# Kernel tuning notes

Hardware: AMD Instinct MI355X
Metric: run time of the kernel (lower is better)

The kernel has to match this reference:

```python
import jax, jax.numpy as jnp
import numpy as np

EPS = 1e-8

def rms_norm(x, scale):
    # norm(2,-1)/sqrt(d); x / (rms + eps) * scale
    d = x.shape[-1]
    norm = jnp.sqrt(jnp.sum(x * x, axis=-1, keepdims=True))
    rms = norm / jnp.sqrt(jnp.asarray(d, x.dtype))
    return scale * (x / (rms + EPS))

def setup_inputs() -> dict:
    key = jax.random.key(0)
    B, N, C, FF = 2, 2048, 1024, 4096
    ks = jax.random.split(key, 12)
    s = 0.02
    return {
        "x":  jax.random.normal(ks[0], (B, N, C), jnp.float32),
        "wq": jax.random.normal(ks[1], (C, C), jnp.float32) * s,
        "bq": jnp.zeros((C,), jnp.float32),
        "wk": jax.random.normal(ks[2], (C, C), jnp.float32) * s,
        "bk": jnp.zeros((C,), jnp.float32),
        "wv": jax.random.normal(ks[3], (C, C), jnp.float32) * s,
        "bv": jnp.zeros((C,), jnp.float32),
        "wo": jax.random.normal(ks[4], (C, C), jnp.float32) * s,
        "bo": jnp.zeros((C,), jnp.float32),
        "scale1": jnp.ones((C,), jnp.float32),
        "scale2": jnp.ones((C,), jnp.float32),
        "w1": jax.random.normal(ks[5], (C, FF), jnp.float32) * s,
        "b1": jnp.zeros((FF,), jnp.float32),
        "w2": jax.random.normal(ks[6], (FF, C), jnp.float32) * s,
        "b2": jnp.zeros((C,), jnp.float32),
    }

def reference(x, wq, bq, wk, bk, wv, bv, wo, bo, scale1, scale2, w1, b1, w2, b2):
    B, N, C = x.shape
    H = 16
    D = C // H

    residual = x
    xn = rms_norm(x, scale1)

    def heads(y):  # [B,N,C] -> [B,H,N,D]
        return y.reshape(B, N, H, D).transpose(0, 2, 1, 3)

    q = heads(xn @ wq + bq)
    k = heads(xn @ wk + bk)
    v = heads(xn @ wv + bv)

    # apply_rotary_pos_emb with cos=sin=1: q' = q - roll(q,1,-1), same for k
    q = q - jnp.roll(q, 1, axis=-1)
    k = k - jnp.roll(k, 1, axis=-1)

    # explicit attention (no causal mask in original)
    scores = jnp.einsum('bhnd,bhmd->bhnm', q, k) / jnp.sqrt(jnp.asarray(D, x.dtype))
    probs = jax.nn.softmax(scores, axis=-1)
    attn = jnp.einsum('bhnm,bhmd->bhnd', probs, v)
    attn = attn.transpose(0, 2, 1, 3).reshape(B, N, C)
    attn = attn @ wo + bo

    x = residual + attn
    residual = x
    xn = rms_norm(x, scale2)
    h = jax.nn.gelu(xn @ w1 + b1, approximate=False)  # torch GELU default = exact
    ffn_out = h @ w2 + b2
    return residual + ffn_out
```

## Files before the change

### kernel.cpp

```cpp
#include <hip/hip_runtime.h>
#include <hip/hip_bf16.h>
#include <math.h>

typedef unsigned short u16;
typedef short s16x8 __attribute__((ext_vector_type(8)));
typedef __bf16 bf16x8v __attribute__((ext_vector_type(8)));
typedef float f32x4 __attribute__((ext_vector_type(4)));
typedef unsigned short u16x4 __attribute__((ext_vector_type(4)));

struct Ptr4 { float* p[4]; };
struct TW6 {
    const float* w[6]; u16* o[6]; int mode[6];
    const float *bq, *bk, *bv; float* bqkv;
};

__device__ __forceinline__ u16 f2b(float f) {
    __hip_bfloat16 h = __float2bfloat16(f);
    return __builtin_bit_cast(u16, h);
}

__device__ __forceinline__ f32x4 mfma16(s16x8 a, s16x8 b, f32x4 c) {
    return __builtin_amdgcn_mfma_f32_16x16x32_bf16(
        __builtin_bit_cast(bf16x8v, a), __builtin_bit_cast(bf16x8v, b), c, 0, 0, 0);
}

__device__ __forceinline__ void gl_lds16(const void* g, void* l) {
    typedef const unsigned int __attribute__((address_space(1))) * gp_t;
    typedef unsigned int __attribute__((address_space(3))) * lp_t;
    __builtin_amdgcn_global_load_lds((gp_t)(unsigned long long)g,
                                     (lp_t)(unsigned int)(unsigned long long)l,
                                     16, 0, 0);
}

__device__ __forceinline__ float gelu_fast(float v) {
    float u = 1.5957691216f * (v + 0.044715f * v * v * v);
    return v / (1.f + __expf(-u));
}

__global__ __launch_bounds__(256) void prep_weights(TW6 io) {
    const int z = blockIdx.z, bx = blockIdx.x, by = blockIdx.y;
    const float* W; u16* Wt; int mode = 0, N_, K_, n0, k0;
    if (z < 4) {
        if (bx >= 32) {
            if (z == 0 && bx < 44 && by == 0) {
                const int i = (bx - 32) * 256 + threadIdx.x;
                const int d = i & 1023;
                const int dp = (d & ~63) | ((d + 63) & 63);
                float v;
                if (i < 1024) v = 0.125f * (io.bq[d] - io.bq[dp]);
                else if (i < 2048) v = io.bk[d] - io.bk[dp];
                else v = io.bv[d];
                io.bqkv[i] = v;
            }
            return;
        }
        W = io.w[z]; Wt = io.o[z]; mode = io.mode[z];
        N_ = 1024; K_ = 1024; n0 = bx * 32; k0 = by * 32;
    } else if (z == 4) {
        W = io.w[4]; Wt = io.o[4]; N_ = 4096; K_ = 1024; n0 = bx * 32; k0 = by * 32;
    } else {
        W = io.w[5]; Wt = io.o[5]; N_ = 1024; K_ = 4096; n0 = by * 32; k0 = bx * 32;
    }
    __shared__ u16 tile[32][33];
    const int tx = threadIdx.x & 31, ty = threadIdx.x >> 5;
    const int n = n0 + tx;
    const int np = (n & ~63) | ((n + 63) & 63);
    const float s = (mode == 1) ? 0.125f : 1.f;
#pragma unroll
    for (int i = 0; i < 32; i += 8) {
        const size_t r = (size_t)(k0 + ty + i) * N_;
        float v = W[r + n];
        if (mode) v = (v - W[r + np]) * s;
        tile[ty + i][tx] = f2b(v);
    }
    __syncthreads();
#pragma unroll
    for (int i = 0; i < 32; i += 8)
        Wt[(size_t)(n0 + ty + i) * K_ + k0 + tx] = tile[tx][ty + i];
}

__global__ __launch_bounds__(256) void transpose_v(const u16* __restrict__ qkv,
                                                   u16* __restrict__ vT) {
    __shared__ u16 tile[32][33];
    const int tx = threadIdx.x & 31, ty = threadIdx.x >> 5;
    const int n0 = blockIdx.x * 32, d0 = blockIdx.y * 32, bh = blockIdx.z;
    const int b = bh >> 4, h = bh & 15;
#pragma unroll
    for (int i = 0; i < 32; i += 8)
        tile[ty + i][tx] =
            qkv[(size_t)(b * 2048 + n0 + ty + i) * 3072 + 2048 + h * 64 + d0 + tx];
    __syncthreads();
#pragma unroll
    for (int i = 0; i < 32; i += 8)
        vT[((size_t)bh * 64 + d0 + ty + i) * 2048 + n0 + tx] = tile[tx][ty + i];
}

__global__ __launch_bounds__(256) void rmsnorm_kernel(const float* __restrict__ x,
                                                      const float* __restrict__ scale,
                                                      u16* __restrict__ out) {
    __shared__ float red[4];
    const int t = threadIdx.x, row = blockIdx.x;
    const float4* xr = (const float4*)(x + (size_t)row * 1024);
    float4 v = xr[t];
    float ss = v.x * v.x + v.y * v.y + v.z * v.z + v.w * v.w;
#pragma unroll
    for (int off = 1; off < 64; off <<= 1) ss += __shfl_xor(ss, off);
    if ((t & 63) == 0) red[t >> 6] = ss;
    __syncthreads();
    float tot = red[0] + red[1] + red[2] + red[3];
    float inv = 1.f / (sqrtf(tot * (1.f / 1024.f)) + 1e-8f);
    const float4* sr = (const float4*)scale;
    float4 s = sr[t];
    u16x4 o;
    o[0] = f2b(v.x * inv * s.x);
    o[1] = f2b(v.y * inv * s.y);
    o[2] = f2b(v.z * inv * s.z);
    o[3] = f2b(v.w * inv * s.w);
    ((u16x4*)(out + (size_t)row * 1024))[t] = o;
}

template <int EPI>
__global__ __launch_bounds__(256) void gemm_kernel(const u16* __restrict__ A,
                                                   const u16* __restrict__ Bt,
                                                   const float* __restrict__ bias,
                                                   const float* __restrict__ resid,
                                                   void* __restrict__ outp,
                                                   int M, int N, int K) {
    __shared__ __align__(16) u16 As[128 * 64];
    __shared__ __align__(16) u16 Bs[128 * 64];
    const int t = threadIdx.x, lane = t & 63;
    const int w = t >> 6, wm = (w >> 1) * 64, wn = (w & 1) * 64;
    const int c = lane & 15, qd = lane >> 4;
    const int n0 = blockIdx.x * 128, m0 = blockIdx.y * 128;

    const int srow = t >> 3;
    const int sch8 = ((t & 7) ^ (srow & 7)) * 8;
    const u16* Ag = A + (size_t)(m0 + srow) * K + sch8;
    const u16* Bg = Bt + (size_t)(n0 + srow) * K + sch8;
    const size_t rstride = (size_t)32 * K;

    f32x4 acc[4][4] = {};
    for (int kt = 0; kt < K; kt += 64) {
        __syncthreads();
#pragma unroll
        for (int g = 0; g < 4; g++) {
            gl_lds16(Ag + g * rstride, &As[t * 8 + g * 2048]);
            gl_lds16(Bg + g * rstride, &Bs[t * 8 + g * 2048]);
        }
        Ag += 64;
        Bg += 64;
        __syncthreads();
#pragma unroll
        for (int s = 0; s < 2; s++) {
            s16x8 a[4], b[4];
#pragma unroll
            for (int im = 0; im < 4; im++)
                a[im] = *(const s16x8*)&As[(wm + im * 16 + c) * 64 +
                                           (((s * 4 + qd) ^ (c & 7)) * 8)];
#pragma unroll
            for (int jn = 0; jn < 4; jn++)
                b[jn] = *(const s16x8*)&Bs[(wn + jn * 16 + c) * 64 +
                                           (((s * 4 + qd) ^ (c & 7)) * 8)];
#pragma unroll
            for (int im = 0; im < 4; im++)
#pragma unroll
                for (int jn = 0; jn < 4; jn++)
                    acc[im][jn] = mfma16(a[im], b[jn], acc[im][jn]);
        }
    }

#pragma unroll
    for (int im = 0; im < 4; im++) {
#pragma unroll
        for (int jn = 0; jn < 4; jn++) {
            const int colg = n0 + wn + jn * 16 + c;
            const float bv = bias[colg];
#pragma unroll
            for (int r = 0; r < 4; r++) {
                const int rowg = m0 + wm + im * 16 + qd * 4 + r;
                const size_t off = (size_t)rowg * N + colg;
                float v = acc[im][jn][r] + bv;
                if (EPI == 0) {
                    ((u16*)outp)[off] = f2b(v);
                } else if (EPI == 1) {
                    ((float*)outp)[off] = v + resid[off];
                } else {
                    ((u16*)outp)[off] = f2b(gelu_fast(v));
                }
            }
        }
    }
}

__global__ __launch_bounds__(256) void gemm_splitk(const u16* __restrict__ A,
                                                   const u16* __restrict__ Bt,
                                                   Ptr4 parts,
                                                   int N, int Ktot, int Kc) {
    __shared__ __align__(16) u16 As[128 * 64];
    __shared__ __align__(16) u16 Bs[128 * 64];
    const int t = threadIdx.x, lane = t & 63;
    const int w = t >> 6, wm = (w >> 1) * 64, wn = (w & 1) * 64;
    const int c = lane & 15, qd = lane >> 4;
    const int n0 = blockIdx.x * 128, m0 = blockIdx.y * 128;
    const int z = blockIdx.z;
    float* out = parts.p[z];

    const int srow = t >> 3;
    const int sch8 = ((t & 7) ^ (srow & 7)) * 8;
    const u16* Ag = A + (size_t)(m0 + srow) * Ktot + z * Kc + sch8;
    const u16* Bg = Bt + (size_t)(n0 + srow) * Ktot + z * Kc + sch8;
    const size_t rstride = (size_t)32 * Ktot;

    f32x4 acc[4][4] = {};
    for (int kt = 0; kt < Kc; kt += 64) {
        __syncthreads();
#pragma unroll
        for (int g = 0; g < 4; g++) {
            gl_lds16(Ag + g * rstride, &As[t * 8 + g * 2048]);
            gl_lds16(Bg + g * rstride, &Bs[t * 8 + g * 2048]);
        }
        Ag += 64;
        Bg += 64;
        __syncthreads();
#pragma unroll
        for (int s = 0; s < 2; s++) {
            s16x8 a[4], b[4];
#pragma unroll
            for (int im = 0; im < 4; im++)
                a[im] = *(const s16x8*)&As[(wm + im * 16 + c) * 64 +
                                           (((s * 4 + qd) ^ (c & 7)) * 8)];
#pragma unroll
            for (int jn = 0; jn < 4; jn++)
                b[jn] = *(const s16x8*)&Bs[(wn + jn * 16 + c) * 64 +
                                           (((s * 4 + qd) ^ (c & 7)) * 8)];
#pragma unroll
            for (int im = 0; im < 4; im++)
#pragma unroll
                for (int jn = 0; jn < 4; jn++)
                    acc[im][jn] = mfma16(a[im], b[jn], acc[im][jn]);
        }
    }

#pragma unroll
    for (int im = 0; im < 4; im++)
#pragma unroll
        for (int jn = 0; jn < 4; jn++) {
            const int colg = n0 + wn + jn * 16 + c;
#pragma unroll
            for (int r = 0; r < 4; r++) {
                const int rowg = m0 + wm + im * 16 + qd * 4 + r;
                out[(size_t)rowg * N + colg] = acc[im][jn][r];
            }
        }
}

template <int S, bool NORM>
__global__ __launch_bounds__(256) void reduce_kernel(Ptr4 parts,
                                                     const float* __restrict__ bias,
                                                     const float* __restrict__ resid,
                                                     const float* __restrict__ scale,
                                                     float* __restrict__ yout,
                                                     u16* __restrict__ xnout) {
    __shared__ float red[4];
    const int t = threadIdx.x, row = blockIdx.x;
    const size_t base = (size_t)row * 1024;
    float4 v = ((const float4*)(resid + base))[t];
    float4 bv = ((const float4*)bias)[t];
    v.x += bv.x; v.y += bv.y; v.z += bv.z; v.w += bv.w;
#pragma unroll
    for (int s = 0; s < S; s++) {
        float4 pv = ((const float4*)(parts.p[s] + base))[t];
        v.x += pv.x; v.y += pv.y; v.z += pv.z; v.w += pv.w;
    }
    ((float4*)(yout + base))[t] = v;
    if (NORM) {
        float ss = v.x * v.x + v.y * v.y + v.z * v.z + v.w * v.w;
#pragma unroll
        for (int off = 1; off < 64; off <<= 1) ss += __shfl_xor(ss, off);
        if ((t & 63) == 0) red[t >> 6] = ss;
        __syncthreads();
        float tot = red[0] + red[1] + red[2] + red[3];
        float inv = 1.f / (sqrtf(tot * (1.f / 1024.f)) + 1e-8f);
        float4 s = ((const float4*)scale)[t];
        u16x4 o;
        o[0] = f2b(v.x * inv * s.x);
        o[1] = f2b(v.y * inv * s.y);
        o[2] = f2b(v.z * inv * s.z);
        o[3] = f2b(v.w * inv * s.w);
        ((u16x4*)(xnout + base))[t] = o;
    }
}

__global__ __launch_bounds__(256, 3) void attn_kernel(const u16* __restrict__ qkv,
                                                      const u16* __restrict__ vT,
                                                      u16* __restrict__ attn) {
    __shared__ __align__(16) u16 Ks[2][64 * 64];
    __shared__ __align__(16) u16 Vs[2][64 * 64];
    __shared__ __align__(16) u16 Ps[4 * 32 * 64];

    const int t = threadIdx.x, lane = t & 63, w = t >> 6;
    const int c = lane & 15, qd = lane >> 4;
    const int bh = blockIdx.y, b = bh >> 4, h = bh & 15;
    const int q0 = blockIdx.x * 128;
    const size_t rowbase = (size_t)b * 2048;

    const u16* kg = qkv + rowbase * 3072 + 1024 + h * 64;
    const u16* vg = vT + (size_t)bh * 64 * 2048;

    const int srow = t >> 3;
    const int sch = (t & 7) ^ (srow & 7);

    const u16* kptr = kg + (size_t)srow * 3072 + sch * 8;
    const u16* vptr = vg + (size_t)srow * 2048 + sch * 8;

    gl_lds16(kptr, &Ks[0][t * 8]);
    gl_lds16(kptr + (size_t)32 * 3072, &Ks[0][2048 + t * 8]);
    gl_lds16(vptr, &Vs[0][t * 8]);
    gl_lds16(vptr + (size_t)32 * 2048, &Vs[0][2048 + t * 8]);

    s16x8 qf[2][2];
    {
        const u16* qg = qkv + (rowbase + q0 + w * 32) * 3072 + h * 64;
#pragma unroll
        for (int im = 0; im < 2; im++)
#pragma unroll
            for (int ks = 0; ks < 2; ks++)
                qf[im][ks] = *(const s16x8*)&qg[(size_t)(im * 16 + c) * 3072 +
                                                ks * 32 + qd * 8];
    }
    __syncthreads();

    float lsum[2][4] = {};
    f32x4 o[2][4] = {};
    u16* Pw = &Ps[w * 32 * 64];

    for (int it = 0; it < 32; it++) {
        const int buf = it & 1;
        const u16* Kb = Ks[buf];
        const u16* Vb = Vs[buf];

        if (it + 1 < 32) {
            u16* Kn = Ks[buf ^ 1];
            u16* Vn = Vs[buf ^ 1];
            const size_t ko = (size_t)(it + 1) * 64 * 3072;
            const size_t vo = (size_t)(it + 1) * 64;
            gl_lds16(kptr + ko, &Kn[t * 8]);
            gl_lds16(kptr + ko + (size_t)32 * 3072, &Kn[2048 + t * 8]);
            gl_lds16(vptr + vo, &Vn[t * 8]);
            gl_lds16(vptr + vo + (size_t)32 * 2048, &Vn[2048 + t * 8]);
        }

        s16x8 kf[2][4], vf[2][4];
#pragma unroll
        for (int ks = 0; ks < 2; ks++)
#pragma unroll
            for (int j = 0; j < 4; j++) {
                const int rrow = j * 16 + c;
                const int sw = ((ks * 4 + qd) ^ (rrow & 7)) * 8;
                kf[ks][j] = *(const s16x8*)&Kb[rrow * 64 + sw];
                vf[ks][j] = *(const s16x8*)&Vb[rrow * 64 + sw];
            }

#pragma unroll
        for (int im = 0; im < 2; im++) {
            f32x4 sc[4] = {};
#pragma unroll
            for (int ks = 0; ks < 2; ks++)
#pragma unroll
                for (int jn = 0; jn < 4; jn++)
                    sc[jn] = mfma16(qf[im][ks], kf[ks][jn], sc[jn]);
#pragma unroll
            for (int r = 0; r < 4; r++) {
                const int prow = im * 16 + qd * 4 + r;
                float s = 0.f;
#pragma unroll
                for (int jn = 0; jn < 4; jn++) {
                    float p = __expf(sc[jn][r]);
                    s += p;
                    Pw[prow * 64 + (((jn * 2 + (c >> 3)) ^ (prow & 7)) * 8) + (c & 7)] =
                        f2b(p);
                }
                lsum[im][r] += s;
            }
        }

#pragma unroll
        for (int im = 0; im < 2; im++)
#pragma unroll
            for (int ks = 0; ks < 2; ks++) {
                s16x8 pf = *(const s16x8*)&Pw[(im * 16 + c) * 64 +
                                              (((ks * 4 + qd) ^ (c & 7)) * 8)];
#pragma unroll
                for (int jd = 0; jd < 4; jd++)
                    o[im][jd] = mfma16(pf, vf[ks][jd], o[im][jd]);
            }
        __syncthreads();
    }

#pragma unroll
    for (int im = 0; im < 2; im++)
#pragma unroll
        for (int r = 0; r < 4; r++)
#pragma unroll
            for (int off2 = 1; off2 < 16; off2 <<= 1)
                lsum[im][r] += __shfl_xor(lsum[im][r], off2);

    const int orow_base = b * 2048 + q0 + w * 32;
#pragma unroll
    for (int im = 0; im < 2; im++)
#pragma unroll
        for (int r = 0; r < 4; r++) {
            const float inv = 1.f / lsum[im][r];
            const int grow = orow_base + im * 16 + qd * 4 + r;
#pragma unroll
            for (int jd = 0; jd < 4; jd++)
                attn[(size_t)grow * 1024 + h * 64 + jd * 16 + c] =
                    f2b(o[im][jd][r] * inv);
        }
}

extern "C" void kernel_launch(void* const* d_in, const int* in_sizes, int n_in,
                              void* d_out, int out_size, void* d_ws, size_t ws_size,
                              hipStream_t stream) {
    const float* x = (const float*)d_in[0];
    const float* wq = (const float*)d_in[1];
    const float* bq = (const float*)d_in[2];
    const float* wk = (const float*)d_in[3];
    const float* bk = (const float*)d_in[4];
    const float* wv = (const float*)d_in[5];
    const float* bv = (const float*)d_in[6];
    const float* wo = (const float*)d_in[7];
    const float* bo = (const float*)d_in[8];
    const float* scale1 = (const float*)d_in[9];
    const float* scale2 = (const float*)d_in[10];
    const float* w1 = (const float*)d_in[11];
    const float* b1 = (const float*)d_in[12];
    const float* w2 = (const float*)d_in[13];
    const float* b2 = (const float*)d_in[14];
    float* out = (float*)d_out;

    char* ws = (char*)d_ws;
    size_t off = 0;
    auto alloc = [&](size_t bytes) -> char* {
        char* p = ws + off;
        off += (bytes + 255) & ~(size_t)255;
        return p;
    };
    u16* wqkvT = (u16*)alloc((size_t)3072 * 1024 * 2);
    u16* woT   = (u16*)alloc((size_t)1024 * 1024 * 2);
    u16* w1T   = (u16*)alloc((size_t)4096 * 1024 * 2);
    u16* w2T   = (u16*)alloc((size_t)1024 * 4096 * 2);
    float* bqkv = (float*)alloc(3072 * 4);
    u16* xn    = (u16*)alloc((size_t)4096 * 1024 * 2);
    u16* qkv   = (u16*)alloc((size_t)4096 * 3072 * 2);
    u16* vT    = (u16*)alloc((size_t)32 * 64 * 2048 * 2);
    u16* attnb = (u16*)alloc((size_t)4096 * 1024 * 2);
    float* y1  = (float*)alloc((size_t)4096 * 1024 * 4);
    u16* hbuf  = (u16*)alloc((size_t)4096 * 4096 * 2);

    const size_t SPLIT = (size_t)4096 * 1024;
    Ptr4 po; po.p[0] = (float*)qkv; po.p[1] = (float*)qkv + SPLIT;
    po.p[2] = nullptr; po.p[3] = nullptr;
    Ptr4 pf; pf.p[0] = (float*)xn; pf.p[1] = (float*)xn + SPLIT;
    pf.p[2] = (float*)xn + 2 * SPLIT; pf.p[3] = (float*)wqkvT;

    dim3 blk(256);

    TW6 tw;
    tw.w[0] = wq; tw.o[0] = wqkvT;                          tw.mode[0] = 1;
    tw.w[1] = wk; tw.o[1] = wqkvT + (size_t)1024 * 1024;    tw.mode[1] = 2;
    tw.w[2] = wv; tw.o[2] = wqkvT + (size_t)2048 * 1024;    tw.mode[2] = 0;
    tw.w[3] = wo; tw.o[3] = woT;                            tw.mode[3] = 0;
    tw.w[4] = w1; tw.o[4] = w1T;                            tw.mode[4] = 0;
    tw.w[5] = w2; tw.o[5] = w2T;                            tw.mode[5] = 0;
    tw.bq = bq; tw.bk = bk; tw.bv = bv; tw.bqkv = bqkv;
    prep_weights<<<dim3(128, 32, 6), blk, 0, stream>>>(tw);

    rmsnorm_kernel<<<4096, blk, 0, stream>>>(x, scale1, xn);
    gemm_kernel<0><<<dim3(24, 32), blk, 0, stream>>>(xn, wqkvT, bqkv, nullptr, qkv, 4096, 3072, 1024);
    transpose_v<<<dim3(64, 2, 32), blk, 0, stream>>>(qkv, vT);
    attn_kernel<<<dim3(16, 32), blk, 0, stream>>>(qkv, vT, attnb);
    gemm_splitk<<<dim3(8, 32, 2), blk, 0, stream>>>(attnb, woT, po, 1024, 1024, 512);
    reduce_kernel<2, true><<<4096, blk, 0, stream>>>(po, bo, x, scale2, y1, xn);
    gemm_kernel<2><<<dim3(32, 32), blk, 0, stream>>>(xn, w1T, b1, nullptr, hbuf, 4096, 4096, 1024);
    gemm_splitk<<<dim3(8, 32, 4), blk, 0, stream>>>(hbuf, w2T, pf, 1024, 4096, 1024);
    reduce_kernel<4, false><<<4096, blk, 0, stream>>>(pf, b2, y1, nullptr, out, nullptr);
}
```

Measured before the change: 369.3 us.

## Shrink attention query tile, use exp2 with folded scale, compute row sums via MFMA

Each attention workgroup now handles 64 query rows (16 per wave) instead of 128, which halves per-wave accumulators and P scratch, raises the occupancy hint to 4, and doubles the grid. The grid is 1D with a remapping so consecutive blocks go to different XCDs (id&7) while keeping heads together. The softmax scale and log2(e) are folded into the Q weights so exp becomes a native exp2. Row sums are accumulated with an extra MFMA against a ones vector instead of scalar adds and shuffles. s_setprio brackets around the MFMA sections aim to favour matrix issue. The trade-off is that K/V tiles are now loaded twice as often per query, and the row sums come from bf16-rounded probabilities.

```diff
diff --git a/kernel.cpp b/kernel.cpp
--- a/kernel.cpp
+++ b/kernel.cpp
@@ -17,6 +17,14 @@
 __device__ __forceinline__ u16 f2b(float f) {
     __hip_bfloat16 h = __float2bfloat16(f);
     return __builtin_bit_cast(u16, h);
+}
+
+__device__ __forceinline__ float exp2_fast(float x) {
+#if __has_builtin(__builtin_amdgcn_exp2f)
+    return __builtin_amdgcn_exp2f(x);
+#else
+    return exp2f(x);
+#endif
 }
 
 __device__ __forceinline__ f32x4 mfma16(s16x8 a, s16x8 b, f32x4 c) {
@@ -36,6 +44,8 @@
     float u = 1.5957691216f * (v + 0.044715f * v * v * v);
     return v / (1.f + __expf(-u));
 }
+
+#define QSCALE 0.1803368801111244f
 
 __global__ __launch_bounds__(256) void prep_weights(TW6 io) {
     const int z = blockIdx.z, bx = blockIdx.x, by = blockIdx.y;
@@ -47,7 +57,7 @@
                 const int d = i & 1023;
                 const int dp = (d & ~63) | ((d + 63) & 63);
                 float v;
-                if (i < 1024) v = 0.125f * (io.bq[d] - io.bq[dp]);
+                if (i < 1024) v = QSCALE * (io.bq[d] - io.bq[dp]);
                 else if (i < 2048) v = io.bk[d] - io.bk[dp];
                 else v = io.bv[d];
                 io.bqkv[i] = v;
@@ -65,7 +75,7 @@
     const int tx = threadIdx.x & 31, ty = threadIdx.x >> 5;
     const int n = n0 + tx;
     const int np = (n & ~63) | ((n + 63) & 63);
-    const float s = (mode == 1) ? 0.125f : 1.f;
+    const float s = (mode == 1) ? QSCALE : 1.f;
 #pragma unroll
     for (int i = 0; i < 32; i += 8) {
         const size_t r = (size_t)(k0 + ty + i) * N_;
@@ -291,17 +301,21 @@
     }
 }
 
-__global__ __launch_bounds__(256, 3) void attn_kernel(const u16* __restrict__ qkv,
+__global__ __launch_bounds__(256, 4) void attn_kernel(const u16* __restrict__ qkv,
                                                       const u16* __restrict__ vT,
                                                       u16* __restrict__ attn) {
     __shared__ __align__(16) u16 Ks[2][64 * 64];
     __shared__ __align__(16) u16 Vs[2][64 * 64];
-    __shared__ __align__(16) u16 Ps[4 * 32 * 64];
+    __shared__ __align__(16) u16 Ps[4 * 16 * 64];
 
     const int t = threadIdx.x, lane = t & 63, w = t >> 6;
     const int c = lane & 15, qd = lane >> 4;
-    const int bh = blockIdx.y, b = bh >> 4, h = bh & 15;
-    const int q0 = blockIdx.x * 128;
+
+    const int id = blockIdx.x;
+    const int logical = (id & 7) * 128 + (id >> 3);
+    const int bh = logical >> 5, qb = logical & 31;
+    const int b = bh >> 4, h = bh & 15;
+    const int q0 = qb * 64;
     const size_t rowbase = (size_t)b * 2048;
 
     const u16* kg = qkv + rowbase * 3072 + 1024 + h * 64;
@@ -318,21 +332,19 @@
     gl_lds16(vptr, &Vs[0][t * 8]);
     gl_lds16(vptr + (size_t)32 * 2048, &Vs[0][2048 + t * 8]);
 
-    s16x8 qf[2][2];
+    s16x8 qf[2];
     {
-        const u16* qg = qkv + (rowbase + q0 + w * 32) * 3072 + h * 64;
-#pragma unroll
-        for (int im = 0; im < 2; im++)
-#pragma unroll
-            for (int ks = 0; ks < 2; ks++)
-                qf[im][ks] = *(const s16x8*)&qg[(size_t)(im * 16 + c) * 3072 +
-                                                ks * 32 + qd * 8];
+        const u16* qg = qkv + (rowbase + q0 + w * 16) * 3072 + h * 64;
+#pragma unroll
+        for (int ks = 0; ks < 2; ks++)
+            qf[ks] = *(const s16x8*)&qg[(size_t)c * 3072 + ks * 32 + qd * 8];
     }
     __syncthreads();
 
-    float lsum[2][4] = {};
-    f32x4 o[2][4] = {};
-    u16* Pw = &Ps[w * 32 * 64];
+    const s16x8 ones = {16256, 16256, 16256, 16256, 16256, 16256, 16256, 16256};
+    f32x4 lsum = {0.f, 0.f, 0.f, 0.f};
+    f32x4 o[4] = {};
+    u16* Pw = &Ps[w * 16 * 64];
 
     for (int it = 0; it < 32; it++) {
         const int buf = it & 1;
@@ -361,62 +373,49 @@
                 vf[ks][j] = *(const s16x8*)&Vb[rrow * 64 + sw];
             }
 
-#pragma unroll
-        for (int im = 0; im < 2; im++) {
-            f32x4 sc[4] = {};
-#pragma unroll
-            for (int ks = 0; ks < 2; ks++)
-#pragma unroll
-                for (int jn = 0; jn < 4; jn++)
-                    sc[jn] = mfma16(qf[im][ks], kf[ks][jn], sc[jn]);
-#pragma unroll
-            for (int r = 0; r < 4; r++) {
-                const int prow = im * 16 + qd * 4 + r;
-                float s = 0.f;
-#pragma unroll
-                for (int jn = 0; jn < 4; jn++) {
-                    float p = __expf(sc[jn][r]);
-                    s += p;
-                    Pw[prow * 64 + (((jn * 2 + (c >> 3)) ^ (prow & 7)) * 8) + (c & 7)] =
-                        f2b(p);
-                }
-                lsum[im][r] += s;
+        f32x4 sc[4] = {};
+        __builtin_amdgcn_s_setprio(1);
+#pragma unroll
+        for (int ks = 0; ks < 2; ks++)
+#pragma unroll
+            for (int jn = 0; jn < 4; jn++)
+                sc[jn] = mfma16(qf[ks], kf[ks][jn], sc[jn]);
+        __builtin_amdgcn_s_setprio(0);
+
+#pragma unroll
+        for (int r = 0; r < 4; r++) {
+            const int prow = qd * 4 + r;
+#pragma unroll
+            for (int jn = 0; jn < 4; jn++) {
+                float p = exp2_fast(sc[jn][r]);
+                Pw[prow * 64 + (((jn * 2 + (c >> 3)) ^ (prow & 7)) * 8) + (c & 7)] =
+                    f2b(p);
             }
         }
 
-#pragma unroll
-        for (int im = 0; im < 2; im++)
-#pragma unroll
-            for (int ks = 0; ks < 2; ks++) {
-                s16x8 pf = *(const s16x8*)&Pw[(im * 16 + c) * 64 +
-                                              (((ks * 4 + qd) ^ (c & 7)) * 8)];
-#pragma unroll
-                for (int jd = 0; jd < 4; jd++)
-                    o[im][jd] = mfma16(pf, vf[ks][jd], o[im][jd]);
-            }
-        __syncthreads();
-    }
-
-#pragma unroll
-    for (int im = 0; im < 2; im++)
-#pragma unroll
-        for (int r = 0; r < 4; r++)
-#pragma unroll
-            for (int off2 = 1; off2 < 16; off2 <<= 1)
-                lsum[im][r] += __shfl_xor(lsum[im][r], off2);
-
-    const int orow_base = b * 2048 + q0 + w * 32;
-#pragma unroll
-    for (int im = 0; im < 2; im++)
-#pragma unroll
-        for (int r = 0; r < 4; r++) {
-            const float inv = 1.f / lsum[im][r];
-            const int grow = orow_base + im * 16 + qd * 4 + r;
+        __builtin_amdgcn_s_setprio(1);
+#pragma unroll
+        for (int ks = 0; ks < 2; ks++) {
+            s16x8 pf = *(const s16x8*)&Pw[c * 64 + (((ks * 4 + qd) ^ (c & 7)) * 8)];
+            lsum = mfma16(pf, ones, lsum);
 #pragma unroll
             for (int jd = 0; jd < 4; jd++)
-                attn[(size_t)grow * 1024 + h * 64 + jd * 16 + c] =
-                    f2b(o[im][jd][r] * inv);
-        }
+                o[jd] = mfma16(pf, vf[ks][jd], o[jd]);
+        }
+        __builtin_amdgcn_s_setprio(0);
+        __syncthreads();
+    }
+
+    const int orow_base = b * 2048 + q0 + w * 16;
+#pragma unroll
+    for (int r = 0; r < 4; r++) {
+        const float inv = 1.f / lsum[r];
+        const int grow = orow_base + qd * 4 + r;
+#pragma unroll
+        for (int jd = 0; jd < 4; jd++)
+            attn[(size_t)grow * 1024 + h * 64 + jd * 16 + c] =
+                f2b(o[jd][r] * inv);
+    }
 }
 
 extern "C" void kernel_launch(void* const* d_in, const int* in_sizes, int n_in,
@@ -479,7 +478,7 @@
     rmsnorm_kernel<<<4096, blk, 0, stream>>>(x, scale1, xn);
     gemm_kernel<0><<<dim3(24, 32), blk, 0, stream>>>(xn, wqkvT, bqkv, nullptr, qkv, 4096, 3072, 1024);
     transpose_v<<<dim3(64, 2, 32), blk, 0, stream>>>(qkv, vT);
-    attn_kernel<<<dim3(16, 32), blk, 0, stream>>>(qkv, vT, attnb);
+    attn_kernel<<<dim3(1024), blk, 0, stream>>>(qkv, vT, attnb);
     gemm_splitk<<<dim3(8, 32, 2), blk, 0, stream>>>(attnb, woT, po, 1024, 1024, 512);
     reduce_kernel<2, true><<<4096, blk, 0, stream>>>(po, bo, x, scale2, y1, xn);
     gemm_kernel<2><<<dim3(32, 32), blk, 0, stream>>>(xn, w1T, b1, nullptr, hbuf, 4096, 4096, 1024);
```

Result: no change. 369.3 us (+0.0%).
